# Optimization experiments

Measured on AMD Instinct MI355X. Metric: run time of the kernel, lower is better.

The kernel has to match this reference:

```python
import jax, jax.numpy as jnp
import numpy as np

N_USERS = 10000
RESERVE = 100
N_TOTAL = N_USERS + RESERVE  # 10100 graph nodes (incl. unknown-user slots)
D = 128                      # user_id_embedding_size
B = 2048                     # batch of user ids
AVG_DEG = 32


def _build_friendship_matrix(rng: np.random.Generator) -> np.ndarray:
    # Dense symmetric friendship matrix with 1.0 on the diagonal (self-loop),
    # mirroring torch.diag(ones) + symmetric weighted edge insertion.
    F = np.zeros((N_TOTAL, N_TOTAL), dtype=np.float32)
    np.fill_diagonal(F, 1.0)
    n_edges = N_USERS * AVG_DEG // 2
    src = rng.integers(0, N_USERS, size=n_edges)
    dst = rng.integers(0, N_USERS, size=n_edges)
    w = rng.uniform(0.1, 1.0, size=n_edges).astype(np.float32)
    F[src, dst] = w
    F[dst, src] = w
    return F


def setup_inputs() -> dict:
    key = jax.random.key(0)
    k_ids, k_emb, k_w, k_b = jax.random.split(key, 4)
    rng = np.random.default_rng(0)
    user_ids = jax.random.randint(k_ids, (B,), 0, N_USERS, dtype=jnp.int32)
    friendship_matrix = jnp.asarray(_build_friendship_matrix(rng))      # (N, N)
    # torch init: embeddings ~ U[0,1); Linear weight/bias ~ U[-1/sqrt(d), 1/sqrt(d)]
    user_id_embeddings = jax.random.uniform(k_emb, (N_TOTAL, D), dtype=jnp.float32)
    bound = 1.0 / np.sqrt(D)
    lin_weight = jax.random.uniform(k_w, (D, D), minval=-bound, maxval=bound, dtype=jnp.float32)
    lin_bias = jax.random.uniform(k_b, (D,), minval=-bound, maxval=bound, dtype=jnp.float32)
    return {
        "user_ids": user_ids,
        "friendship_matrix": friendship_matrix,
        "user_id_embeddings": user_id_embeddings,
        "lin_weight": lin_weight,
        "lin_bias": lin_bias,
    }


def reference(user_ids, friendship_matrix, user_id_embeddings, lin_weight, lin_bias):
    # Per user: friends = F[uid]; aggregated = sum_n friends[n] * E[n]
    # Vectorized over the batch: gather rows of F, then one GEMM with E.
    friends = friendship_matrix[user_ids]                 # (B, N)
    aggregated = friends @ user_id_embeddings             # (B, D)
    # torch.nn.Linear: x @ W^T + b
    return aggregated @ lin_weight.T + lin_bias           # (B, D)
```

## Files before the change

kernel.cpp:

```cpp
#include <hip/hip_runtime.h>


#define NTOT 10100
#define NV4  2525
#define DIM  128
#define CAP  1024
#define TPB  512
#define NGRP 4

__global__ __launch_bounds__(TPB) void friendship_kernel(
    const int*   __restrict__ uids,
    const float* __restrict__ F,
    const float* __restrict__ E,
    const float* __restrict__ W,
    const float* __restrict__ bias,
    float*       __restrict__ out)
{
    __shared__ int   s_idx[CAP];
    __shared__ float s_w[CAP];
    __shared__ int   s_cnt;
    __shared__ float s_red[TPB];
    __shared__ float s_agg[DIM];
    __shared__ float s_out[DIM];

    const int row = blockIdx.x;
    const int tid = threadIdx.x;
    const int uid = uids[row];
    const float* Frow = F + (size_t)uid * NTOT;

    if (tid == 0) s_cnt = 0;
    __syncthreads();

    const float4* Frow4 = (const float4*)Frow;
    for (int i = tid; i < NV4; i += TPB) {
        float4 v = Frow4[i];
        int n = i * 4;
        bool ba = v.x != 0.0f, bb = v.y != 0.0f, bc = v.z != 0.0f, bd = v.w != 0.0f;
        int  m  = (int)ba + (int)bb + (int)bc + (int)bd;
        if (m) {
            int p = atomicAdd(&s_cnt, m);
            if (p + m <= CAP) {
                if (ba) { s_idx[p] = n;     s_w[p] = v.x; ++p; }
                if (bb) { s_idx[p] = n + 1; s_w[p] = v.y; ++p; }
                if (bc) { s_idx[p] = n + 2; s_w[p] = v.z; ++p; }
                if (bd) { s_idx[p] = n + 3; s_w[p] = v.w; ++p; }
            }
        }
    }
    __syncthreads();

    const int cnt = s_cnt;
    const int d   = tid & (DIM - 1);
    const int g   = tid >> 7;

    float acc = 0.0f;
    if (cnt <= CAP) {
        int k = g;
        for (; k + 3 * NGRP < cnt; k += 4 * NGRP) {
            int   n0 = s_idx[k],            n1 = s_idx[k +     NGRP];
            int   n2 = s_idx[k + 2 * NGRP], n3 = s_idx[k + 3 * NGRP];
            float w0 = s_w[k],              w1 = s_w[k +     NGRP];
            float w2 = s_w[k + 2 * NGRP],   w3 = s_w[k + 3 * NGRP];
            acc += w0 * E[(size_t)n0 * DIM + d];
            acc += w1 * E[(size_t)n1 * DIM + d];
            acc += w2 * E[(size_t)n2 * DIM + d];
            acc += w3 * E[(size_t)n3 * DIM + d];
        }
        for (; k < cnt; k += NGRP)
            acc += s_w[k] * E[(size_t)s_idx[k] * DIM + d];
    } else {
        for (int n = g; n < NTOT; n += NGRP)
            acc += Frow[n] * E[(size_t)n * DIM + d];
    }
    s_red[tid] = acc;
    __syncthreads();
    if (tid < DIM)
        s_agg[tid] = s_red[tid] + s_red[tid + DIM] + s_red[tid + 2 * DIM] + s_red[tid + 3 * DIM];
    __syncthreads();

    const float4* W4 = (const float4*)W;
    #pragma unroll
    for (int q = 0; q < 8; ++q) {
        int i4 = tid + TPB * q;
        float4 wv = W4[i4];
        int dd = (i4 & 31) * 4;
        float p = wv.x * s_agg[dd]     + wv.y * s_agg[dd + 1]
                + wv.z * s_agg[dd + 2] + wv.w * s_agg[dd + 3];
        p += __shfl_xor(p, 16);
        p += __shfl_xor(p, 8);
        p += __shfl_xor(p, 4);
        p += __shfl_xor(p, 2);
        p += __shfl_xor(p, 1);
        if ((tid & 31) == 0) s_out[i4 >> 5] = p;
    }
    __syncthreads();
    if (tid < DIM)
        out[(size_t)row * DIM + tid] = bias[tid] + s_out[tid];
}

extern "C" void kernel_launch(void* const* d_in, const int* in_sizes, int n_in,
                              void* d_out, int out_size, void* d_ws, size_t ws_size,
                              hipStream_t stream) {
    const int*   uids = (const int*)  d_in[0];
    const float* F    = (const float*)d_in[1];
    const float* E    = (const float*)d_in[2];
    const float* W    = (const float*)d_in[3];
    const float* bias = (const float*)d_in[4];
    float*       out  = (float*)d_out;

    const int B = in_sizes[0];
    friendship_kernel<<<B, TPB, 0, stream>>>(uids, F, E, W, bias, out);
}
```

Baseline: 30.70 us.

## Process four batch rows per block and vectorize embedding gather

Each block now handles four user rows instead of one: 128 threads per row scan the friendship row, then all 16 wavefront groups gather embedding rows with float4 loads for every row. Each W float4 load is reused across the four rows in the linear layer. The sparse-list capacity is reduced to 256, so rows with more nonzeros take the slower dense path. Grid size drops by four, and launch bounds request higher occupancy.

```diff
diff --git a/kernel.cpp b/kernel.cpp
--- a/kernel.cpp
+++ b/kernel.cpp
@@ -4,78 +4,95 @@
 #define NTOT 10100
 #define NV4  2525
 #define DIM  128
-#define CAP  1024
+#define CAP  256
 #define TPB  512
-#define NGRP 4
+#define R    4
 
-__global__ __launch_bounds__(TPB) void friendship_kernel(
+__global__ __launch_bounds__(TPB, 4) void friendship_kernel(
     const int*   __restrict__ uids,
     const float* __restrict__ F,
     const float* __restrict__ E,
     const float* __restrict__ W,
     const float* __restrict__ bias,
-    float*       __restrict__ out)
+    float*       __restrict__ out,
+    int B)
 {
-    __shared__ int   s_idx[CAP];
-    __shared__ float s_w[CAP];
-    __shared__ int   s_cnt;
-    __shared__ float s_red[TPB];
-    __shared__ float s_agg[DIM];
-    __shared__ float s_out[DIM];
+    __shared__ int   s_idx[R][CAP];
+    __shared__ float s_w[R][CAP];
+    __shared__ int   s_cnt[R];
+    __shared__ float s_red[R][16][DIM];
+    __shared__ float s_agg[R][DIM];
+    __shared__ float s_out[R][DIM];
 
-    const int row = blockIdx.x;
-    const int tid = threadIdx.x;
-    const int uid = uids[row];
-    const float* Frow = F + (size_t)uid * NTOT;
+    const int tid  = threadIdx.x;
+    const int base = blockIdx.x * R;
 
-    if (tid == 0) s_cnt = 0;
+    if (tid < R) s_cnt[tid] = 0;
     __syncthreads();
 
-    const float4* Frow4 = (const float4*)Frow;
-    for (int i = tid; i < NV4; i += TPB) {
-        float4 v = Frow4[i];
-        int n = i * 4;
-        bool ba = v.x != 0.0f, bb = v.y != 0.0f, bc = v.z != 0.0f, bd = v.w != 0.0f;
-        int  m  = (int)ba + (int)bb + (int)bc + (int)bd;
-        if (m) {
-            int p = atomicAdd(&s_cnt, m);
-            if (p + m <= CAP) {
-                if (ba) { s_idx[p] = n;     s_w[p] = v.x; ++p; }
-                if (bb) { s_idx[p] = n + 1; s_w[p] = v.y; ++p; }
-                if (bc) { s_idx[p] = n + 2; s_w[p] = v.z; ++p; }
-                if (bd) { s_idx[p] = n + 3; s_w[p] = v.w; ++p; }
+    const int tr = tid >> 7;
+    const int lr = tid & 127;
+    const bool row_ok = (base + tr) < B;
+    if (row_ok) {
+        const int uid = uids[base + tr];
+        const float4* Frow4 = (const float4*)(F + (size_t)uid * NTOT);
+        for (int i = lr; i < NV4; i += 128) {
+            float4 v = Frow4[i];
+            int n = i * 4;
+            bool ba = v.x != 0.0f, bb = v.y != 0.0f, bc = v.z != 0.0f, bd = v.w != 0.0f;
+            int  m  = (int)ba + (int)bb + (int)bc + (int)bd;
+            if (m) {
+                int p = atomicAdd(&s_cnt[tr], m);
+                if (p + m <= CAP) {
+                    if (ba) { s_idx[tr][p] = n;     s_w[tr][p] = v.x; ++p; }
+                    if (bb) { s_idx[tr][p] = n + 1; s_w[tr][p] = v.y; ++p; }
+                    if (bc) { s_idx[tr][p] = n + 2; s_w[tr][p] = v.z; ++p; }
+                    if (bd) { s_idx[tr][p] = n + 3; s_w[tr][p] = v.w; ++p; }
+                }
             }
         }
     }
     __syncthreads();
 
-    const int cnt = s_cnt;
-    const int d   = tid & (DIM - 1);
-    const int g   = tid >> 7;
+    const int g = tid >> 5;
+    const int l = tid & 31;
+    float4 acc[R];
+    #pragma unroll
+    for (int r = 0; r < R; ++r) acc[r] = make_float4(0.f, 0.f, 0.f, 0.f);
 
-    float acc = 0.0f;
-    if (cnt <= CAP) {
-        int k = g;
-        for (; k + 3 * NGRP < cnt; k += 4 * NGRP) {
-            int   n0 = s_idx[k],            n1 = s_idx[k +     NGRP];
-            int   n2 = s_idx[k + 2 * NGRP], n3 = s_idx[k + 3 * NGRP];
-            float w0 = s_w[k],              w1 = s_w[k +     NGRP];
-            float w2 = s_w[k + 2 * NGRP],   w3 = s_w[k + 3 * NGRP];
-            acc += w0 * E[(size_t)n0 * DIM + d];
-            acc += w1 * E[(size_t)n1 * DIM + d];
-            acc += w2 * E[(size_t)n2 * DIM + d];
-            acc += w3 * E[(size_t)n3 * DIM + d];
+    #pragma unroll
+    for (int r = 0; r < R; ++r) {
+        if (base + r >= B) break;
+        const int cnt = s_cnt[r];
+        if (cnt <= CAP) {
+            for (int k = g; k < cnt; k += 16) {
+                int   n = s_idx[r][k];
+                float w = s_w[r][k];
+                float4 ev = *(const float4*)(E + (size_t)n * DIM + l * 4);
+                acc[r].x += w * ev.x; acc[r].y += w * ev.y;
+                acc[r].z += w * ev.z; acc[r].w += w * ev.w;
+            }
+        } else {
+            const float* Fr = F + (size_t)uids[base + r] * NTOT;
+            for (int n = g; n < NTOT; n += 16) {
+                float w = Fr[n];
+                float4 ev = *(const float4*)(E + (size_t)n * DIM + l * 4);
+                acc[r].x += w * ev.x; acc[r].y += w * ev.y;
+                acc[r].z += w * ev.z; acc[r].w += w * ev.w;
+            }
         }
-        for (; k < cnt; k += NGRP)
-            acc += s_w[k] * E[(size_t)s_idx[k] * DIM + d];
-    } else {
-        for (int n = g; n < NTOT; n += NGRP)
-            acc += Frow[n] * E[(size_t)n * DIM + d];
     }
-    s_red[tid] = acc;
+    #pragma unroll
+    for (int r = 0; r < R; ++r)
+        *(float4*)&s_red[r][g][l * 4] = acc[r];
     __syncthreads();
-    if (tid < DIM)
-        s_agg[tid] = s_red[tid] + s_red[tid + DIM] + s_red[tid + 2 * DIM] + s_red[tid + 3 * DIM];
+
+    {
+        float sum = 0.0f;
+        #pragma unroll
+        for (int gg = 0; gg < 16; ++gg) sum += s_red[tr][gg][lr];
+        s_agg[tr][lr] = sum;
+    }
     __syncthreads();
 
     const float4* W4 = (const float4*)W;
@@ -83,19 +100,23 @@
     for (int q = 0; q < 8; ++q) {
         int i4 = tid + TPB * q;
         float4 wv = W4[i4];
+        int j  = i4 >> 5;
         int dd = (i4 & 31) * 4;
-        float p = wv.x * s_agg[dd]     + wv.y * s_agg[dd + 1]
-                + wv.z * s_agg[dd + 2] + wv.w * s_agg[dd + 3];
-        p += __shfl_xor(p, 16);
-        p += __shfl_xor(p, 8);
-        p += __shfl_xor(p, 4);
-        p += __shfl_xor(p, 2);
-        p += __shfl_xor(p, 1);
-        if ((tid & 31) == 0) s_out[i4 >> 5] = p;
+        #pragma unroll
+        for (int r = 0; r < R; ++r) {
+            float4 ag = *(const float4*)&s_agg[r][dd];
+            float p = wv.x * ag.x + wv.y * ag.y + wv.z * ag.z + wv.w * ag.w;
+            p += __shfl_xor(p, 16);
+            p += __shfl_xor(p, 8);
+            p += __shfl_xor(p, 4);
+            p += __shfl_xor(p, 2);
+            p += __shfl_xor(p, 1);
+            if ((tid & 31) == 0) s_out[r][j] = p;
+        }
     }
     __syncthreads();
-    if (tid < DIM)
-        out[(size_t)row * DIM + tid] = bias[tid] + s_out[tid];
+    if (row_ok)
+        out[(size_t)(base + tr) * DIM + lr] = bias[lr] + s_out[tr][lr];
 }
 
 extern "C" void kernel_launch(void* const* d_in, const int* in_sizes, int n_in,
@@ -109,5 +130,6 @@
     float*       out  = (float*)d_out;
 
     const int B = in_sizes[0];
-    friendship_kernel<<<B, TPB, 0, stream>>>(uids, F, E, W, bias, out);
+    const int grid = (B + R - 1) / R;
+    friendship_kernel<<<grid, TPB, 0, stream>>>(uids, F, E, W, bias, out, B);
 }
```

Result: slower. 31.66 us (+3.1%).

## Split aggregation and linear into two kernels; vectorize neighbor gather with float4

Applied to the files above, without the earlier changes.

Splits the fused kernel into a scan+aggregate kernel that writes per-row aggregates to workspace, and a separate linear kernel that processes 8 rows per block so each W load is reused across rows. The gather now uses 16 groups of 32 lanes, each lane loading a float4 of E, with a fixed unrolled 64-neighbor prefix padded with zero weights. The sparse buffer cap drops from 1024 to 256. This adds a second launch and a global round trip for the aggregates, and rows with more than 256 nonzeros fall back to a dense scan.

```diff
diff --git a/kernel.cpp b/kernel.cpp
--- a/kernel.cpp
+++ b/kernel.cpp
@@ -4,24 +4,21 @@
 #define NTOT 10100
 #define NV4  2525
 #define DIM  128
-#define CAP  1024
+#define CAP  256
+#define KMAX 64
 #define TPB  512
-#define NGRP 4
+#define RB   8
 
-__global__ __launch_bounds__(TPB) void friendship_kernel(
+__global__ __launch_bounds__(TPB) void scan_agg_kernel(
     const int*   __restrict__ uids,
     const float* __restrict__ F,
     const float* __restrict__ E,
-    const float* __restrict__ W,
-    const float* __restrict__ bias,
-    float*       __restrict__ out)
+    float*       __restrict__ agg)
 {
     __shared__ int   s_idx[CAP];
     __shared__ float s_w[CAP];
     __shared__ int   s_cnt;
-    __shared__ float s_red[TPB];
-    __shared__ float s_agg[DIM];
-    __shared__ float s_out[DIM];
+    __shared__ float s_red[16][DIM];
 
     const int row = blockIdx.x;
     const int tid = threadIdx.x;
@@ -50,32 +47,66 @@
     __syncthreads();
 
     const int cnt = s_cnt;
-    const int d   = tid & (DIM - 1);
-    const int g   = tid >> 7;
+    for (int t = cnt + tid; t < KMAX; t += TPB) { s_idx[t] = 0; s_w[t] = 0.0f; }
+    __syncthreads();
 
-    float acc = 0.0f;
+    const int g = tid >> 5;
+    const int l = tid & 31;
+    float4 acc = make_float4(0.f, 0.f, 0.f, 0.f);
+
     if (cnt <= CAP) {
-        int k = g;
-        for (; k + 3 * NGRP < cnt; k += 4 * NGRP) {
-            int   n0 = s_idx[k],            n1 = s_idx[k +     NGRP];
-            int   n2 = s_idx[k + 2 * NGRP], n3 = s_idx[k + 3 * NGRP];
-            float w0 = s_w[k],              w1 = s_w[k +     NGRP];
-            float w2 = s_w[k + 2 * NGRP],   w3 = s_w[k + 3 * NGRP];
-            acc += w0 * E[(size_t)n0 * DIM + d];
-            acc += w1 * E[(size_t)n1 * DIM + d];
-            acc += w2 * E[(size_t)n2 * DIM + d];
-            acc += w3 * E[(size_t)n3 * DIM + d];
+        #pragma unroll
+        for (int t = 0; t < KMAX / 16; ++t) {
+            int   k = g + 16 * t;
+            int   n = s_idx[k];
+            float w = s_w[k];
+            float4 ev = *(const float4*)(E + (size_t)n * DIM + l * 4);
+            acc.x += w * ev.x; acc.y += w * ev.y;
+            acc.z += w * ev.z; acc.w += w * ev.w;
         }
-        for (; k < cnt; k += NGRP)
-            acc += s_w[k] * E[(size_t)s_idx[k] * DIM + d];
+        for (int k = g + KMAX; k < cnt; k += 16) {
+            int   n = s_idx[k];
+            float w = s_w[k];
+            float4 ev = *(const float4*)(E + (size_t)n * DIM + l * 4);
+            acc.x += w * ev.x; acc.y += w * ev.y;
+            acc.z += w * ev.z; acc.w += w * ev.w;
+        }
     } else {
-        for (int n = g; n < NTOT; n += NGRP)
-            acc += Frow[n] * E[(size_t)n * DIM + d];
+        for (int n = g; n < NTOT; n += 16) {
+            float w = Frow[n];
+            float4 ev = *(const float4*)(E + (size_t)n * DIM + l * 4);
+            acc.x += w * ev.x; acc.y += w * ev.y;
+            acc.z += w * ev.z; acc.w += w * ev.w;
+        }
     }
-    s_red[tid] = acc;
+    *(float4*)&s_red[g][l * 4] = acc;
     __syncthreads();
-    if (tid < DIM)
-        s_agg[tid] = s_red[tid] + s_red[tid + DIM] + s_red[tid + 2 * DIM] + s_red[tid + 3 * DIM];
+
+    if (tid < DIM) {
+        float sum = 0.0f;
+        #pragma unroll
+        for (int gg = 0; gg < 16; ++gg) sum += s_red[gg][tid];
+        agg[(size_t)row * DIM + tid] = sum;
+    }
+}
+
+__global__ __launch_bounds__(TPB) void linear_kernel(
+    const float* __restrict__ agg,
+    const float* __restrict__ W,
+    const float* __restrict__ bias,
+    float*       __restrict__ out,
+    int B)
+{
+    __shared__ float s_agg[RB][DIM];
+    __shared__ float s_out[RB][DIM];
+
+    const int tid  = threadIdx.x;
+    const int base = blockIdx.x * RB;
+
+    for (int i = tid; i < RB * DIM; i += TPB) {
+        int r = i >> 7;
+        ((float*)s_agg)[i] = (base + r < B) ? agg[(size_t)base * DIM + i] : 0.0f;
+    }
     __syncthreads();
 
     const float4* W4 = (const float4*)W;
@@ -83,19 +114,27 @@
     for (int q = 0; q < 8; ++q) {
         int i4 = tid + TPB * q;
         float4 wv = W4[i4];
+        int j  = i4 >> 5;
         int dd = (i4 & 31) * 4;
-        float p = wv.x * s_agg[dd]     + wv.y * s_agg[dd + 1]
-                + wv.z * s_agg[dd + 2] + wv.w * s_agg[dd + 3];
-        p += __shfl_xor(p, 16);
-        p += __shfl_xor(p, 8);
-        p += __shfl_xor(p, 4);
-        p += __shfl_xor(p, 2);
-        p += __shfl_xor(p, 1);
-        if ((tid & 31) == 0) s_out[i4 >> 5] = p;
+        #pragma unroll
+        for (int r = 0; r < RB; ++r) {
+            float4 ag = *(const float4*)&s_agg[r][dd];
+            float p = wv.x * ag.x + wv.y * ag.y + wv.z * ag.z + wv.w * ag.w;
+            p += __shfl_xor(p, 16);
+            p += __shfl_xor(p, 8);
+            p += __shfl_xor(p, 4);
+            p += __shfl_xor(p, 2);
+            p += __shfl_xor(p, 1);
+            if ((tid & 31) == 0) s_out[r][j] = p;
+        }
     }
     __syncthreads();
-    if (tid < DIM)
-        out[(size_t)row * DIM + tid] = bias[tid] + s_out[tid];
+
+    for (int i = tid; i < RB * DIM; i += TPB) {
+        int r = i >> 7, d = i & 127;
+        if (base + r < B)
+            out[(size_t)(base + r) * DIM + d] = bias[d] + s_out[r][d];
+    }
 }
 
 extern "C" void kernel_launch(void* const* d_in, const int* in_sizes, int n_in,
@@ -107,7 +146,9 @@
     const float* W    = (const float*)d_in[3];
     const float* bias = (const float*)d_in[4];
     float*       out  = (float*)d_out;
+    float*       agg  = (float*)d_ws;
 
     const int B = in_sizes[0];
-    friendship_kernel<<<B, TPB, 0, stream>>>(uids, F, E, W, bias, out);
+    scan_agg_kernel<<<B, TPB, 0, stream>>>(uids, F, E, agg);
+    linear_kernel<<<(B + RB - 1) / RB, TPB, 0, stream>>>(agg, W, bias, out, B);
 }
```

After: 38.60 us. 25.7% more time.

## Halve block size, vectorize embedding gather with float4, unroll row scan

Applied to the files above, without the earlier changes.

The block shrinks from 512 to 256 threads with a launch-bounds occupancy hint, and the neighbor cap drops from 1024 to 256. The embedding gather now has 8 groups of 32 lanes each load a float4 per neighbor, replacing 4 groups doing scalar loads. The friendship-row scan is unrolled by two so more loads are in flight per thread. The aim is fewer, wider memory transactions and higher occupancy, but rows with more than 256 neighbors fall back to the slow dense path over the whole row.

```diff
diff --git a/kernel.cpp b/kernel.cpp
--- a/kernel.cpp
+++ b/kernel.cpp
@@ -4,11 +4,10 @@
 #define NTOT 10100
 #define NV4  2525
 #define DIM  128
-#define CAP  1024
-#define TPB  512
-#define NGRP 4
+#define CAP  256
+#define TPB  256
 
-__global__ __launch_bounds__(TPB) void friendship_kernel(
+__global__ __launch_bounds__(TPB, 6) void friendship_kernel(
     const int*   __restrict__ uids,
     const float* __restrict__ F,
     const float* __restrict__ E,
@@ -19,7 +18,7 @@
     __shared__ int   s_idx[CAP];
     __shared__ float s_w[CAP];
     __shared__ int   s_cnt;
-    __shared__ float s_red[TPB];
+    __shared__ float s_red[8][DIM];
     __shared__ float s_agg[DIM];
     __shared__ float s_out[DIM];
 
@@ -32,7 +31,40 @@
     __syncthreads();
 
     const float4* Frow4 = (const float4*)Frow;
-    for (int i = tid; i < NV4; i += TPB) {
+    int i = tid;
+    for (; i + TPB < NV4; i += 2 * TPB) {
+        float4 v0 = Frow4[i];
+        float4 v1 = Frow4[i + TPB];
+        {
+            int n = i * 4;
+            bool ba = v0.x != 0.0f, bb = v0.y != 0.0f, bc = v0.z != 0.0f, bd = v0.w != 0.0f;
+            int  m  = (int)ba + (int)bb + (int)bc + (int)bd;
+            if (m) {
+                int p = atomicAdd(&s_cnt, m);
+                if (p + m <= CAP) {
+                    if (ba) { s_idx[p] = n;     s_w[p] = v0.x; ++p; }
+                    if (bb) { s_idx[p] = n + 1; s_w[p] = v0.y; ++p; }
+                    if (bc) { s_idx[p] = n + 2; s_w[p] = v0.z; ++p; }
+                    if (bd) { s_idx[p] = n + 3; s_w[p] = v0.w; ++p; }
+                }
+            }
+        }
+        {
+            int n = (i + TPB) * 4;
+            bool ba = v1.x != 0.0f, bb = v1.y != 0.0f, bc = v1.z != 0.0f, bd = v1.w != 0.0f;
+            int  m  = (int)ba + (int)bb + (int)bc + (int)bd;
+            if (m) {
+                int p = atomicAdd(&s_cnt, m);
+                if (p + m <= CAP) {
+                    if (ba) { s_idx[p] = n;     s_w[p] = v1.x; ++p; }
+                    if (bb) { s_idx[p] = n + 1; s_w[p] = v1.y; ++p; }
+                    if (bc) { s_idx[p] = n + 2; s_w[p] = v1.z; ++p; }
+                    if (bd) { s_idx[p] = n + 3; s_w[p] = v1.w; ++p; }
+                }
+            }
+        }
+    }
+    for (; i < NV4; i += TPB) {
         float4 v = Frow4[i];
         int n = i * 4;
         bool ba = v.x != 0.0f, bb = v.y != 0.0f, bc = v.z != 0.0f, bd = v.w != 0.0f;
@@ -50,48 +82,59 @@
     __syncthreads();
 
     const int cnt = s_cnt;
-    const int d   = tid & (DIM - 1);
-    const int g   = tid >> 7;
+    const int g = tid >> 5;
+    const int l = tid & 31;
 
-    float acc = 0.0f;
+    float4 acc = make_float4(0.f, 0.f, 0.f, 0.f);
     if (cnt <= CAP) {
         int k = g;
-        for (; k + 3 * NGRP < cnt; k += 4 * NGRP) {
-            int   n0 = s_idx[k],            n1 = s_idx[k +     NGRP];
-            int   n2 = s_idx[k + 2 * NGRP], n3 = s_idx[k + 3 * NGRP];
-            float w0 = s_w[k],              w1 = s_w[k +     NGRP];
-            float w2 = s_w[k + 2 * NGRP],   w3 = s_w[k + 3 * NGRP];
-            acc += w0 * E[(size_t)n0 * DIM + d];
-            acc += w1 * E[(size_t)n1 * DIM + d];
-            acc += w2 * E[(size_t)n2 * DIM + d];
-            acc += w3 * E[(size_t)n3 * DIM + d];
+        for (; k + 8 < cnt; k += 16) {
+            int   n0 = s_idx[k];     float w0 = s_w[k];
+            int   n1 = s_idx[k + 8]; float w1 = s_w[k + 8];
+            float4 e0 = *(const float4*)(E + (size_t)n0 * DIM + l * 4);
+            float4 e1 = *(const float4*)(E + (size_t)n1 * DIM + l * 4);
+            acc.x += w0 * e0.x; acc.y += w0 * e0.y; acc.z += w0 * e0.z; acc.w += w0 * e0.w;
+            acc.x += w1 * e1.x; acc.y += w1 * e1.y; acc.z += w1 * e1.z; acc.w += w1 * e1.w;
         }
-        for (; k < cnt; k += NGRP)
-            acc += s_w[k] * E[(size_t)s_idx[k] * DIM + d];
+        for (; k < cnt; k += 8) {
+            int   n = s_idx[k];
+            float w = s_w[k];
+            float4 ev = *(const float4*)(E + (size_t)n * DIM + l * 4);
+            acc.x += w * ev.x; acc.y += w * ev.y; acc.z += w * ev.z; acc.w += w * ev.w;
+        }
     } else {
-        for (int n = g; n < NTOT; n += NGRP)
-            acc += Frow[n] * E[(size_t)n * DIM + d];
+        for (int n = g; n < NTOT; n += 8) {
+            float w = Frow[n];
+            float4 ev = *(const float4*)(E + (size_t)n * DIM + l * 4);
+            acc.x += w * ev.x; acc.y += w * ev.y; acc.z += w * ev.z; acc.w += w * ev.w;
+        }
     }
-    s_red[tid] = acc;
+    *(float4*)&s_red[g][l * 4] = acc;
     __syncthreads();
-    if (tid < DIM)
-        s_agg[tid] = s_red[tid] + s_red[tid + DIM] + s_red[tid + 2 * DIM] + s_red[tid + 3 * DIM];
+
+    if (tid < DIM) {
+        float sum = 0.0f;
+        #pragma unroll
+        for (int gg = 0; gg < 8; ++gg) sum += s_red[gg][tid];
+        s_agg[tid] = sum;
+    }
     __syncthreads();
 
     const float4* W4 = (const float4*)W;
     #pragma unroll
-    for (int q = 0; q < 8; ++q) {
+    for (int q = 0; q < 16; ++q) {
         int i4 = tid + TPB * q;
         float4 wv = W4[i4];
+        int j  = i4 >> 5;
         int dd = (i4 & 31) * 4;
-        float p = wv.x * s_agg[dd]     + wv.y * s_agg[dd + 1]
-                + wv.z * s_agg[dd + 2] + wv.w * s_agg[dd + 3];
+        float4 ag = *(const float4*)&s_agg[dd];
+        float p = wv.x * ag.x + wv.y * ag.y + wv.z * ag.z + wv.w * ag.w;
         p += __shfl_xor(p, 16);
         p += __shfl_xor(p, 8);
         p += __shfl_xor(p, 4);
         p += __shfl_xor(p, 2);
         p += __shfl_xor(p, 1);
-        if ((tid & 31) == 0) s_out[i4 >> 5] = p;
+        if ((tid & 31) == 0) s_out[j] = p;
     }
     __syncthreads();
     if (tid < DIM)
```

Result: no change. 30.26 us (-1.4%).
